# Kernel tuning notes

Hardware: AMD Instinct MI355X
Metric: run time of the kernel (lower is better)

Reference implementation:

```python
import jax, jax.numpy as jnp
import numpy as np

B, N, M = 16, 100000, 9  # batch, point_num, max_neighbor_num (slot 0 = self)


def setup_inputs() -> dict:
    key = jax.random.key(0)
    k1, k2, k3 = jax.random.split(key, 3)
    gt_pc = jax.random.normal(k1, (B, N, 3), dtype=jnp.float32)
    predict_pc = gt_pc + 0.1 * jax.random.normal(k2, (B, N, 3), dtype=jnp.float32)
    # neighbor ids in [0, N]; index N is the padding row (appended zero point)
    nb = jax.random.randint(k3, (N, M), 0, N + 1)
    nb = nb.at[:, 0].set(jnp.arange(N))  # slot 0 is the center vertex itself
    # degree = number of real (non-padding) neighbors
    neighbor_num = (nb[:, 1:] < N).sum(axis=1).astype(jnp.float32)
    return {
        "gt_pc": gt_pc,
        "predict_pc": predict_pc,
        "neighbor_id_lstlst": nb,
        "neighbor_num_lst": neighbor_num,
    }


def _laplacian(pc, neighbor_id_lstlst, neighbor_num_lst):
    # pc: [B, N, 3]; append a zero point so padding index N gathers zeros
    b = pc.shape[0]
    pc_ext = jnp.concatenate([pc, jnp.zeros((b, 1, 3), pc.dtype)], axis=1)  # [B, N+1, 3]
    g = pc_ext[:, neighbor_id_lstlst]  # [B, N, M, 3] gather of self + neighbors
    center = g[:, :, 0] * neighbor_num_lst[None, :, None]  # degree * x_i
    return center - g[:, :, 1:].sum(axis=2)  # deg*x_i - sum_j x_j


def reference(gt_pc, predict_pc, neighbor_id_lstlst, neighbor_num_lst):
    gt_lap = _laplacian(gt_pc, neighbor_id_lstlst, neighbor_num_lst)
    pr_lap = _laplacian(predict_pc, neighbor_id_lstlst, neighbor_num_lst)
    return jnp.abs(gt_lap - pr_lap).mean()
```

## Files before the change

### kernel.cpp

```cpp
#include <hip/hip_runtime.h>
#include <hip/hip_fp16.h>


#define NT 256
#define TI 256
#define Q  4

typedef float f32x4 __attribute__((ext_vector_type(4)));

union H4 {
  uint2 u;
  __half2 h[2];
};

__global__ __launch_bounds__(NT) void k1_diff_pack(
    const float* __restrict__ gt, const float* __restrict__ pr,
    uint2* __restrict__ dq, float* __restrict__ out, int N) {
  __shared__ float sm[4][3 * TI + 1];
  const int t4 = blockIdx.x & 3;
  const int chunk = blockIdx.x >> 2;
  const int i0 = chunk * TI;
  const int ni = min(TI, N - i0);
  const int nf = 3 * ni;
  const int tid = threadIdx.x;

#pragma unroll
  for (int k = 0; k < (4 * 3 * TI) / (4 * NT); k++) {
    int f4 = tid + k * NT;
    int bs = f4 / (3 * TI / 4);
    int o4 = f4 - bs * (3 * TI / 4);
    int off = o4 * 4;
    size_t gbase = ((size_t)(t4 * 4 + bs) * N + i0) * 3;
    if (off + 4 <= nf) {
      f32x4 gv = __builtin_nontemporal_load((const f32x4*)(gt + gbase + off));
      f32x4 pv = __builtin_nontemporal_load((const f32x4*)(pr + gbase + off));
      sm[bs][off + 0] = gv.x - pv.x;
      sm[bs][off + 1] = gv.y - pv.y;
      sm[bs][off + 2] = gv.z - pv.z;
      sm[bs][off + 3] = gv.w - pv.w;
    } else {
#pragma unroll
      for (int c = 0; c < 4; c++) {
        int o = off + c;
        float v = 0.0f;
        if (o < nf) v = gt[gbase + o] - pr[gbase + o];
        sm[bs][o] = v;
      }
    }
  }
  __syncthreads();

#pragma unroll
  for (int k = 0; k < (4 * TI) / NT; k++) {
    int el = tid + k * NT;
    int il = el >> 2;
    int bs = el & 3;
    if (il < ni) {
      float x = sm[bs][il * 3 + 0];
      float y = sm[bs][il * 3 + 1];
      float z = sm[bs][il * 3 + 2];
      H4 o;
      o.h[0] = __floats2half2_rn(x, y);
      o.h[1] = __floats2half2_rn(z, 0.0f);
      dq[((size_t)t4 * (N + 1) + (i0 + il)) * 4 + bs] = o.u;
    }
  }

  if (chunk == 0) {
    if (tid < 4) {
      uint2 z; z.x = 0u; z.y = 0u;
      dq[((size_t)t4 * (N + 1) + N) * 4 + tid] = z;
    }
    if (t4 == 0 && tid == 4) *out = 0.0f;
  }
}

__device__ __forceinline__ void unpack(uint2 v, float& x, float& y, float& z) {
  H4 c; c.u = v;
  float2 xy = __half22float2(c.h[0]);
  x = xy.x; y = xy.y;
  z = __half2float(__low2half(c.h[1]));
}

__global__ __launch_bounds__(NT) void k2_lap_loss(
    const uint2* __restrict__ dq, const int* __restrict__ nb,
    const float* __restrict__ nn, float* __restrict__ out, int N,
    float scale) {
  const int t4 = blockIdx.x & 3;
  const int chunk = blockIdx.x >> 2;
  const int g = threadIdx.x >> 2;
  const int bs = threadIdx.x & 3;
  const uint2* dqt = dq + (size_t)t4 * (N + 1) * 4 + bs;
  const int ibase = chunk * (64 * Q) + g;

  int ii[Q]; bool val[Q];
#pragma unroll
  for (int q = 0; q < Q; q++) {
    int i = ibase + q * 64;
    val[q] = (i < N);
    ii[q] = val[q] ? i : 0;
  }

  int idx[Q][8];
#pragma unroll
  for (int q = 0; q < Q; q++) {
    const int* r = nb + (size_t)ii[q] * 9 + 1;
#pragma unroll
    for (int j = 0; j < 8; j++) idx[q][j] = __builtin_nontemporal_load(r + j);
  }
  float w[Q]; uint2 c[Q];
#pragma unroll
  for (int q = 0; q < Q; q++) {
    w[q] = __builtin_nontemporal_load(nn + ii[q]);
    c[q] = dqt[(size_t)ii[q] * 4];
  }
  uint2 v[Q][8];
#pragma unroll
  for (int q = 0; q < Q; q++) {
#pragma unroll
    for (int j = 0; j < 8; j++) v[q][j] = dqt[(size_t)idx[q][j] * 4];
  }

  float s = 0.0f;
#pragma unroll
  for (int q = 0; q < Q; q++) {
    float ax, ay, az;
    unpack(c[q], ax, ay, az);
    ax *= w[q]; ay *= w[q]; az *= w[q];
#pragma unroll
    for (int j = 0; j < 8; j++) {
      float x, y, z; unpack(v[q][j], x, y, z);
      ax -= x; ay -= y; az -= z;
    }
    float term = fabsf(ax) + fabsf(ay) + fabsf(az);
    s += val[q] ? term : 0.0f;
  }

#pragma unroll
  for (int off = 32; off > 0; off >>= 1) s += __shfl_down(s, off);
  __shared__ float smr[NT / 64];
  int lane = threadIdx.x & 63, wv = threadIdx.x >> 6;
  if (lane == 0) smr[wv] = s;
  __syncthreads();
  if (threadIdx.x == 0) {
    float tt = 0.0f;
#pragma unroll
    for (int k = 0; k < NT / 64; k++) tt += smr[k];
    atomicAdd(out, tt * scale);
  }
}

__global__ void k0_zero(float* __restrict__ out) {
  if (threadIdx.x == 0) *out = 0.0f;
}

__global__ __launch_bounds__(NT) void k2_direct(
    const float* __restrict__ gt, const float* __restrict__ pr,
    const int* __restrict__ nb, const float* __restrict__ nn,
    float* __restrict__ out, int N, int K, int B, float scale) {
  int u = blockIdx.x * NT + threadIdx.x;
  float s = 0.0f;
  if (u < B * N) {
    int b = u / N;
    int i = u - b * N;
    size_t cidx = ((size_t)b * N + i) * 3;
    float w = nn[i];
    float ax = (gt[cidx] - pr[cidx]) * w;
    float ay = (gt[cidx + 1] - pr[cidx + 1]) * w;
    float az = (gt[cidx + 2] - pr[cidx + 2]) * w;
    const int* row = nb + (size_t)i * (K + 1) + 1;
    for (int j = 0; j < K; j++) {
      int idx = row[j];
      if (idx < N) {
        size_t p = ((size_t)b * N + idx) * 3;
        ax -= (gt[p] - pr[p]);
        ay -= (gt[p + 1] - pr[p + 1]);
        az -= (gt[p + 2] - pr[p + 2]);
      }
    }
    s = fabsf(ax) + fabsf(ay) + fabsf(az);
  }
#pragma unroll
  for (int off = 32; off > 0; off >>= 1) s += __shfl_down(s, off);
  __shared__ float smr[NT / 64];
  int lane = threadIdx.x & 63, wv = threadIdx.x >> 6;
  if (lane == 0) smr[wv] = s;
  __syncthreads();
  if (threadIdx.x == 0) {
    float tt = 0.0f;
#pragma unroll
    for (int k = 0; k < NT / 64; k++) tt += smr[k];
    atomicAdd(out, tt * scale);
  }
}

extern "C" void kernel_launch(void* const* d_in, const int* in_sizes, int n_in,
                              void* d_out, int out_size, void* d_ws, size_t ws_size,
                              hipStream_t stream) {
  const float* gt = (const float*)d_in[0];
  const float* pr = (const float*)d_in[1];
  const int*   nb = (const int*)d_in[2];
  const float* nn = (const float*)d_in[3];
  int N = in_sizes[3];
  int M = in_sizes[2] / N;
  int K = M - 1;
  int B = in_sizes[0] / (3 * N);

  float scale = 1.0f / ((float)B * (float)N * 3.0f);
  size_t need = (size_t)(N + 1) * 4 * 4 * sizeof(uint2);

  if (K == 8 && B == 16 && (N % 4) == 0 && ws_size >= need) {
    uint2* dq = (uint2*)d_ws;

    int nchunk1 = (N + TI - 1) / TI;
    k1_diff_pack<<<4 * nchunk1, NT, 0, stream>>>(gt, pr, dq, (float*)d_out, N);

    int nchunk2 = (N + 64 * Q - 1) / (64 * Q);
    k2_lap_loss<<<4 * nchunk2, NT, 0, stream>>>(dq, nb, nn, (float*)d_out, N,
                                                scale);
  } else {
    k0_zero<<<1, 64, 0, stream>>>((float*)d_out);
    int b2 = (B * N + NT - 1) / NT;
    k2_direct<<<b2, NT, 0, stream>>>(gt, pr, nb, nn, (float*)d_out, N, K, B,
                                     scale);
  }
}
```

Measured before the change: 113.0 us.

## Pack all 16 batches per point into one 128-byte row for gathers

Changes the workspace layout so that each point stores all 16 batch differences in fp16 as 8 uint4 entries. One neighbor gather then fetches a full contiguous 128-byte row, instead of 4 separate 32-byte segments from 4 batch-group planes. The gather kernel now has 8 threads per point, each covering 2 batches, and each thread handles 2 points. This replaces the previous 4 points per thread across 4 batches. The aim is to read each neighbor index once for all batches and to use full cache lines. In exchange each thread issues fewer independent loads, so there is less memory-level parallelism per thread, and the pack kernel's shared tile grows.

```diff
diff --git a/kernel.cpp b/kernel.cpp
--- a/kernel.cpp
+++ b/kernel.cpp
@@ -3,8 +3,7 @@
 
 
 #define NT 256
-#define TI 256
-#define Q  4
+#define TI 128
 
 typedef float f32x4 __attribute__((ext_vector_type(4)));
 
@@ -13,24 +12,28 @@
   __half2 h[2];
 };
 
+union U4 {
+  uint4 u;
+  __half2 h[4];
+};
+
 __global__ __launch_bounds__(NT) void k1_diff_pack(
     const float* __restrict__ gt, const float* __restrict__ pr,
-    uint2* __restrict__ dq, float* __restrict__ out, int N) {
-  __shared__ float sm[4][3 * TI + 1];
-  const int t4 = blockIdx.x & 3;
-  const int chunk = blockIdx.x >> 2;
+    uint4* __restrict__ d, float* __restrict__ out, int N) {
+  __shared__ float sm[16][3 * TI + 1];
+  const int chunk = blockIdx.x;
   const int i0 = chunk * TI;
   const int ni = min(TI, N - i0);
   const int nf = 3 * ni;
   const int tid = threadIdx.x;
 
 #pragma unroll
-  for (int k = 0; k < (4 * 3 * TI) / (4 * NT); k++) {
+  for (int k = 0; k < (16 * 3 * TI) / (4 * NT); k++) {
     int f4 = tid + k * NT;
     int bs = f4 / (3 * TI / 4);
     int o4 = f4 - bs * (3 * TI / 4);
     int off = o4 * 4;
-    size_t gbase = ((size_t)(t4 * 4 + bs) * N + i0) * 3;
+    size_t gbase = ((size_t)bs * N + i0) * 3;
     if (off + 4 <= nf) {
       f32x4 gv = __builtin_nontemporal_load((const f32x4*)(gt + gbase + off));
       f32x4 pv = __builtin_nontemporal_load((const f32x4*)(pr + gbase + off));
@@ -51,90 +54,92 @@
   __syncthreads();
 
 #pragma unroll
-  for (int k = 0; k < (4 * TI) / NT; k++) {
+  for (int k = 0; k < (TI * 8) / NT; k++) {
     int el = tid + k * NT;
-    int il = el >> 2;
-    int bs = el & 3;
+    int il = el >> 3;
+    int bp = el & 7;
     if (il < ni) {
-      float x = sm[bs][il * 3 + 0];
-      float y = sm[bs][il * 3 + 1];
-      float z = sm[bs][il * 3 + 2];
-      H4 o;
-      o.h[0] = __floats2half2_rn(x, y);
-      o.h[1] = __floats2half2_rn(z, 0.0f);
-      dq[((size_t)t4 * (N + 1) + (i0 + il)) * 4 + bs] = o.u;
+      int ba = 2 * bp, bb = 2 * bp + 1;
+      U4 o;
+      o.h[0] = __floats2half2_rn(sm[ba][il * 3 + 0], sm[ba][il * 3 + 1]);
+      o.h[1] = __floats2half2_rn(sm[ba][il * 3 + 2], 0.0f);
+      o.h[2] = __floats2half2_rn(sm[bb][il * 3 + 0], sm[bb][il * 3 + 1]);
+      o.h[3] = __floats2half2_rn(sm[bb][il * 3 + 2], 0.0f);
+      d[(size_t)(i0 + il) * 8 + bp] = o.u;
     }
   }
 
   if (chunk == 0) {
-    if (tid < 4) {
-      uint2 z; z.x = 0u; z.y = 0u;
-      dq[((size_t)t4 * (N + 1) + N) * 4 + tid] = z;
-    }
-    if (t4 == 0 && tid == 4) *out = 0.0f;
-  }
-}
-
-__device__ __forceinline__ void unpack(uint2 v, float& x, float& y, float& z) {
-  H4 c; c.u = v;
-  float2 xy = __half22float2(c.h[0]);
-  x = xy.x; y = xy.y;
-  z = __half2float(__low2half(c.h[1]));
+    if (tid < 8) {
+      uint4 z; z.x = z.y = z.z = z.w = 0u;
+      d[(size_t)N * 8 + tid] = z;
+    }
+    if (tid == 8) *out = 0.0f;
+  }
+}
+
+__device__ __forceinline__ void acc_sub(const U4& c, float& ax, float& ay,
+                                        float& az, float& bx, float& by,
+                                        float& bz) {
+  float2 xy0 = __half22float2(c.h[0]);
+  float2 xy1 = __half22float2(c.h[2]);
+  ax -= xy0.x; ay -= xy0.y; az -= __half2float(__low2half(c.h[1]));
+  bx -= xy1.x; by -= xy1.y; bz -= __half2float(__low2half(c.h[3]));
 }
 
 __global__ __launch_bounds__(NT) void k2_lap_loss(
-    const uint2* __restrict__ dq, const int* __restrict__ nb,
+    const uint4* __restrict__ dp, const int* __restrict__ nb,
     const float* __restrict__ nn, float* __restrict__ out, int N,
     float scale) {
-  const int t4 = blockIdx.x & 3;
-  const int chunk = blockIdx.x >> 2;
-  const int g = threadIdx.x >> 2;
-  const int bs = threadIdx.x & 3;
-  const uint2* dqt = dq + (size_t)t4 * (N + 1) * 4 + bs;
-  const int ibase = chunk * (64 * Q) + g;
-
-  int ii[Q]; bool val[Q];
-#pragma unroll
-  for (int q = 0; q < Q; q++) {
-    int i = ibase + q * 64;
-    val[q] = (i < N);
-    ii[q] = val[q] ? i : 0;
-  }
-
-  int idx[Q][8];
-#pragma unroll
-  for (int q = 0; q < Q; q++) {
-    const int* r = nb + (size_t)ii[q] * 9 + 1;
-#pragma unroll
-    for (int j = 0; j < 8; j++) idx[q][j] = __builtin_nontemporal_load(r + j);
-  }
-  float w[Q]; uint2 c[Q];
-#pragma unroll
-  for (int q = 0; q < Q; q++) {
-    w[q] = __builtin_nontemporal_load(nn + ii[q]);
-    c[q] = dqt[(size_t)ii[q] * 4];
-  }
-  uint2 v[Q][8];
-#pragma unroll
-  for (int q = 0; q < Q; q++) {
-#pragma unroll
-    for (int j = 0; j < 8; j++) v[q][j] = dqt[(size_t)idx[q][j] * 4];
-  }
+  const int f = blockIdx.x * NT + threadIdx.x;
+  const int g = f >> 3;
+  const int bp = f & 7;
+  const bool val = (g < (N >> 1));
+  const int i0 = val ? g * 2 : 0;
+  const int i1 = i0 + 1;
+  const uint4* row = dp + bp;
+
+  int ia[8], ib[8];
+#pragma unroll
+  for (int j = 0; j < 8; j++) {
+    ia[j] = __builtin_nontemporal_load(nb + (size_t)i0 * 9 + 1 + j);
+    ib[j] = __builtin_nontemporal_load(nb + (size_t)i1 * 9 + 1 + j);
+  }
+  float w0 = __builtin_nontemporal_load(nn + i0);
+  float w1 = __builtin_nontemporal_load(nn + i1);
+  U4 c0, c1;
+  c0.u = row[(size_t)i0 * 8];
+  c1.u = row[(size_t)i1 * 8];
+  U4 v0[8], v1[8];
+#pragma unroll
+  for (int j = 0; j < 8; j++) v0[j].u = row[(size_t)ia[j] * 8];
+#pragma unroll
+  for (int j = 0; j < 8; j++) v1[j].u = row[(size_t)ib[j] * 8];
 
   float s = 0.0f;
-#pragma unroll
-  for (int q = 0; q < Q; q++) {
-    float ax, ay, az;
-    unpack(c[q], ax, ay, az);
-    ax *= w[q]; ay *= w[q]; az *= w[q];
-#pragma unroll
-    for (int j = 0; j < 8; j++) {
-      float x, y, z; unpack(v[q][j], x, y, z);
-      ax -= x; ay -= y; az -= z;
-    }
-    float term = fabsf(ax) + fabsf(ay) + fabsf(az);
-    s += val[q] ? term : 0.0f;
-  }
+  {
+    float2 xy0 = __half22float2(c0.h[0]);
+    float2 xy1 = __half22float2(c0.h[2]);
+    float ax = xy0.x * w0, ay = xy0.y * w0;
+    float az = __half2float(__low2half(c0.h[1])) * w0;
+    float bx = xy1.x * w0, by = xy1.y * w0;
+    float bz = __half2float(__low2half(c0.h[3])) * w0;
+#pragma unroll
+    for (int j = 0; j < 8; j++) acc_sub(v0[j], ax, ay, az, bx, by, bz);
+    s += fabsf(ax) + fabsf(ay) + fabsf(az) + fabsf(bx) + fabsf(by) + fabsf(bz);
+  }
+  {
+    float2 xy0 = __half22float2(c1.h[0]);
+    float2 xy1 = __half22float2(c1.h[2]);
+    float ax = xy0.x * w1, ay = xy0.y * w1;
+    float az = __half2float(__low2half(c1.h[1])) * w1;
+    float bx = xy1.x * w1, by = xy1.y * w1;
+    float bz = __half2float(__low2half(c1.h[3])) * w1;
+#pragma unroll
+    for (int j = 0; j < 8; j++) acc_sub(v1[j], ax, ay, az, bx, by, bz);
+    s += fabsf(ax) + fabsf(ay) + fabsf(az) + fabsf(bx) + fabsf(by) + fabsf(bz);
+  }
+  s = val ? s : 0.0f;
 
 #pragma unroll
   for (int off = 32; off > 0; off >>= 1) s += __shfl_down(s, off);
@@ -207,17 +212,17 @@
   int B = in_sizes[0] / (3 * N);
 
   float scale = 1.0f / ((float)B * (float)N * 3.0f);
-  size_t need = (size_t)(N + 1) * 4 * 4 * sizeof(uint2);
-
-  if (K == 8 && B == 16 && (N % 4) == 0 && ws_size >= need) {
-    uint2* dq = (uint2*)d_ws;
-
-    int nchunk1 = (N + TI - 1) / TI;
-    k1_diff_pack<<<4 * nchunk1, NT, 0, stream>>>(gt, pr, dq, (float*)d_out, N);
-
-    int nchunk2 = (N + 64 * Q - 1) / (64 * Q);
-    k2_lap_loss<<<4 * nchunk2, NT, 0, stream>>>(dq, nb, nn, (float*)d_out, N,
-                                                scale);
+  size_t need = (size_t)(N + 1) * 8 * sizeof(uint4);
+
+  if (K == 8 && B == 16 && (N % 4) == 0 && N >= 2 && ws_size >= need) {
+    uint4* d = (uint4*)d_ws;
+
+    int b1 = (N + TI - 1) / TI;
+    k1_diff_pack<<<b1, NT, 0, stream>>>(gt, pr, d, (float*)d_out, N);
+
+    int pairs = N / 2;
+    int b2 = ((size_t)pairs * 8 + NT - 1) / NT;
+    k2_lap_loss<<<b2, NT, 0, stream>>>(d, nb, nn, (float*)d_out, N, scale);
   } else {
     k0_zero<<<1, 64, 0, stream>>>((float*)d_out);
     int b2 = (B * N + NT - 1) / NT;
```

Result: no change. 112.9 us (-0.1%).
